# Kernel tuning notes

Hardware: AMD Instinct MI355X
Metric: run time of the kernel (lower is better)

The kernel has to match this reference:

```python
import jax, jax.numpy as jnp
import numpy as np

WEIGHT_CE = 1.0
WEIGHT_DICE = 1.0
EPS = 1e-10
SMOOTH = 1e-5


def setup_inputs() -> dict:
    key = jax.random.key(0)
    k1, k2 = jax.random.split(key)
    B, N, H, W, D = 2, 8, 128, 128, 128
    logits = jax.random.normal(k1, (B, N, H, W, D), dtype=jnp.float32)
    pred = jax.nn.softmax(logits, axis=1)  # module expects softmaxed preds
    target = jax.random.randint(k2, (B, 1, H, W, D), 0, N, dtype=jnp.int32)
    return {"pred": pred, "target": target}


def reference(pred, target):
    # pred: (B, N, H, W, D) softmax probs; target: (B, 1, H, W, D) int labels
    B, N = pred.shape[0], pred.shape[1]
    t = target[:, 0]  # (B, H, W, D)

    # --- CE part (faithful to the original's cross-batch one-hot bug) ---
    # loss[b2, hwd] = -sum_b sum_c 1[t[b2,hwd]==c] * log(pred[b,c,hwd]+eps)
    logp_sum = jnp.sum(jnp.log(pred + EPS), axis=0)  # (N, H, W, D)
    gathered = jnp.take_along_axis(
        jnp.broadcast_to(logp_sum[None], (B,) + logp_sum.shape),
        t[:, None], axis=1)[:, 0]  # (B, H, W, D)
    celoss = -jnp.mean(gathered) / B

    # --- MONAI DiceLoss(softmax=False, to_onehot_y=True), defaults ---
    oh = (t[:, None] == jnp.arange(N, dtype=t.dtype)[None, :, None, None, None]).astype(pred.dtype)  # (B,N,H,W,D)
    inter = jnp.sum(oh * pred, axis=(2, 3, 4))   # (B, N)
    ground_o = jnp.sum(oh, axis=(2, 3, 4))       # (B, N)
    pred_o = jnp.sum(pred, axis=(2, 3, 4))       # (B, N)
    dice = jnp.mean(1.0 - (2.0 * inter + SMOOTH) / (ground_o + pred_o + SMOOTH))

    return WEIGHT_CE * celoss + WEIGHT_DICE * dice
```

## Files before the change

### kernel.cpp

```cpp
#include <hip/hip_runtime.h>

#define S_VOX (128*128*128)
#define QV (S_VOX/4)
#define EPSF 1e-10f
#define SMOOTHF 1e-5f

#define NACC 49

__device__ __forceinline__ float wave_reduce(float v) {
#pragma unroll
    for (int off = 32; off > 0; off >>= 1)
        v += __shfl_down(v, off, 64);
    return v;
}

__global__ __launch_bounds__(256) void dice_main(const float* __restrict__ pred,
                                                 const int* __restrict__ tgt,
                                                 float* __restrict__ ws) {
    const float4* p4 = (const float4*)pred;
    const int4*   t4 = (const int4*)tgt;

    float ce = 0.f;
    float inter[2][8];
    float po[2][8];
    int   gc[2][8];
#pragma unroll
    for (int b = 0; b < 2; b++)
#pragma unroll
        for (int n = 0; n < 8; n++) { inter[b][n] = 0.f; po[b][n] = 0.f; gc[b][n] = 0; }

    const int tid    = blockIdx.x * blockDim.x + threadIdx.x;
    const int stride = gridDim.x * blockDim.x;

    for (int q = tid; q < QV; q += stride) {
        const int4 t0 = t4[q];
        const int4 t1 = t4[QV + q];
#pragma unroll
        for (int n = 0; n < 8; n++) {
            const float4 a = p4[n * QV + q];
            const float4 b = p4[(8 + n) * QV + q];

            po[0][n] += (a.x + a.y) + (a.z + a.w);
            po[1][n] += (b.x + b.y) + (b.z + b.w);

#define VOXEL(pa, pb, ta, tb)                                              \
            {                                                              \
                float lg = __logf((pa) + EPSF) + __logf((pb) + EPSF);      \
                int m0 = ((ta) == n);                                      \
                int m1 = ((tb) == n);                                      \
                ce += lg * (float)(m0 + m1);                               \
                inter[0][n] += m0 ? (pa) : 0.f;                            \
                inter[1][n] += m1 ? (pb) : 0.f;                            \
                gc[0][n] += m0;                                            \
                gc[1][n] += m1;                                            \
            }
            VOXEL(a.x, b.x, t0.x, t1.x)
            VOXEL(a.y, b.y, t0.y, t1.y)
            VOXEL(a.z, b.z, t0.z, t1.z)
            VOXEL(a.w, b.w, t0.w, t1.w)
#undef VOXEL
        }
    }

    float acc[NACC];
    acc[0] = ce;
#pragma unroll
    for (int b = 0; b < 2; b++)
#pragma unroll
        for (int n = 0; n < 8; n++) {
            acc[1  + b * 8 + n] = inter[b][n];
            acc[17 + b * 8 + n] = (float)gc[b][n];
            acc[33 + b * 8 + n] = po[b][n];
        }

    __shared__ float red[4][NACC];
    const int lane = threadIdx.x & 63;
    const int wave = threadIdx.x >> 6;
#pragma unroll
    for (int i = 0; i < NACC; i++) {
        float v = wave_reduce(acc[i]);
        if (lane == 0) red[wave][i] = v;
    }
    __syncthreads();
    if (threadIdx.x < NACC) {
        float s = red[0][threadIdx.x] + red[1][threadIdx.x] +
                  red[2][threadIdx.x] + red[3][threadIdx.x];
        atomicAdd(&ws[threadIdx.x], s);
    }
}

__global__ void dice_finalize(const float* __restrict__ ws, float* __restrict__ out) {
    const int i = threadIdx.x;
    float term = 0.f;
    if (i < 16) {
        float inter = ws[1 + i];
        float g     = ws[17 + i];
        float p     = ws[33 + i];
        term = 1.0f - (2.0f * inter + SMOOTHF) / (g + p + SMOOTHF);
    }
    term = wave_reduce(term);
    if (i == 0) {
        float celoss = -ws[0] / (4.0f * (float)S_VOX);
        out[0] = celoss + term * (1.0f / 16.0f);
    }
}

extern "C" void kernel_launch(void* const* d_in, const int* in_sizes, int n_in,
                              void* d_out, int out_size, void* d_ws, size_t ws_size,
                              hipStream_t stream) {
    const float* pred = (const float*)d_in[0];
    const int*   tgt  = (const int*)d_in[1];
    float* ws  = (float*)d_ws;
    float* out = (float*)d_out;

    hipMemsetAsync(ws, 0, NACC * sizeof(float), stream);
    dice_main<<<1024, 256, 0, stream>>>(pred, tgt, ws);
    dice_finalize<<<1, 64, 0, stream>>>(ws, out);
}
```

Before: 228.4 us.

## Select gathered probabilities before log, one voxel-quad per thread, fuse finalize

Result: slower. 543.6 us (+138.1%).

```diff
diff --git a/kernel.cpp b/kernel.cpp
--- a/kernel.cpp
+++ b/kernel.cpp
@@ -4,104 +4,108 @@
 #define QV (S_VOX/4)
 #define EPSF 1e-10f
 #define SMOOTHF 1e-5f
+#define NACC 49
+#define NBLK 2048
+#define LN2F 0.69314718056f
 
-#define NACC 49
 
-__device__ __forceinline__ float wave_reduce(float v) {
-#pragma unroll
-    for (int off = 32; off > 0; off >>= 1)
-        v += __shfl_down(v, off, 64);
-    return v;
-}
-
-__global__ __launch_bounds__(256) void dice_main(const float* __restrict__ pred,
-                                                 const int* __restrict__ tgt,
-                                                 float* __restrict__ ws) {
+__global__ __launch_bounds__(256, 2) void dice_main(const float* __restrict__ pred,
+                                                    const int* __restrict__ tgt,
+                                                    float* __restrict__ ws,
+                                                    float* __restrict__ out) {
     const float4* p4 = (const float4*)pred;
     const int4*   t4 = (const int4*)tgt;
+    const int q = blockIdx.x * 256 + threadIdx.x;
 
-    float ce = 0.f;
-    float inter[2][8];
-    float po[2][8];
-    int   gc[2][8];
+    const int4 T0 = t4[q];
+    const int4 T1 = t4[QV + q];
+    float4 A[8], B[8];
 #pragma unroll
-    for (int b = 0; b < 2; b++)
+    for (int n = 0; n < 8; n++) A[n] = p4[n * QV + q];
 #pragma unroll
-        for (int n = 0; n < 8; n++) { inter[b][n] = 0.f; po[b][n] = 0.f; gc[b][n] = 0; }
+    for (int n = 0; n < 8; n++) B[n] = p4[(8 + n) * QV + q];
 
-    const int tid    = blockIdx.x * blockDim.x + threadIdx.x;
-    const int stride = gridDim.x * blockDim.x;
+    float i0[8], i1[8], g0[8], g1[8], po0[8], po1[8];
+    float s00x = A[0].x, s00y = A[0].y, s00z = A[0].z, s00w = A[0].w;
+    float s01x = B[0].x, s01y = B[0].y, s01z = B[0].z, s01w = B[0].w;
+    float s10x = A[0].x, s10y = A[0].y, s10z = A[0].z, s10w = A[0].w;
+    float s11x = B[0].x, s11y = B[0].y, s11z = B[0].z, s11w = B[0].w;
 
-    for (int q = tid; q < QV; q += stride) {
-        const int4 t0 = t4[q];
-        const int4 t1 = t4[QV + q];
 #pragma unroll
-        for (int n = 0; n < 8; n++) {
-            const float4 a = p4[n * QV + q];
-            const float4 b = p4[(8 + n) * QV + q];
+    for (int n = 0; n < 8; n++) {
+        const float4 a = A[n];
+        const float4 b = B[n];
+        po0[n] = (a.x + a.y) + (a.z + a.w);
+        po1[n] = (b.x + b.y) + (b.z + b.w);
 
-            po[0][n] += (a.x + a.y) + (a.z + a.w);
-            po[1][n] += (b.x + b.y) + (b.z + b.w);
+        float ii0 = 0.f, ii1 = 0.f, gg0 = 0.f, gg1 = 0.f;
+#define VOX(c)                                                          \
+        {                                                               \
+            const bool m0 = (T0.c == n);                                \
+            const bool m1 = (T1.c == n);                                \
+            if (n > 0) {                                                \
+                s00##c = m0 ? a.c : s00##c;                             \
+                s01##c = m0 ? b.c : s01##c;                             \
+                s10##c = m1 ? a.c : s10##c;                             \
+                s11##c = m1 ? b.c : s11##c;                             \
+            }                                                           \
+            ii0 += m0 ? a.c : 0.f;                                      \
+            ii1 += m1 ? b.c : 0.f;                                      \
+            gg0 += m0 ? 1.f : 0.f;                                      \
+            gg1 += m1 ? 1.f : 0.f;                                      \
+        }
+        VOX(x) VOX(y) VOX(z) VOX(w)
+#undef VOX
+        i0[n] = ii0; i1[n] = ii1; g0[n] = gg0; g1[n] = gg1;
+    }
 
-#define VOXEL(pa, pb, ta, tb)                                              \
-            {                                                              \
-                float lg = __logf((pa) + EPSF) + __logf((pb) + EPSF);      \
-                int m0 = ((ta) == n);                                      \
-                int m1 = ((tb) == n);                                      \
-                ce += lg * (float)(m0 + m1);                               \
-                inter[0][n] += m0 ? (pa) : 0.f;                            \
-                inter[1][n] += m1 ? (pb) : 0.f;                            \
-                gc[0][n] += m0;                                            \
-                gc[1][n] += m1;                                            \
-            }
-            VOXEL(a.x, b.x, t0.x, t1.x)
-            VOXEL(a.y, b.y, t0.y, t1.y)
-            VOXEL(a.z, b.z, t0.z, t1.z)
-            VOXEL(a.w, b.w, t0.w, t1.w)
-#undef VOXEL
-        }
-    }
+    const float ce = LN2F *
+        ( (__log2f(s00x + EPSF) + __log2f(s01x + EPSF) + __log2f(s10x + EPSF) + __log2f(s11x + EPSF))
+        + (__log2f(s00y + EPSF) + __log2f(s01y + EPSF) + __log2f(s10y + EPSF) + __log2f(s11y + EPSF))
+        + (__log2f(s00z + EPSF) + __log2f(s01z + EPSF) + __log2f(s10z + EPSF) + __log2f(s11z + EPSF))
+        + (__log2f(s00w + EPSF) + __log2f(s01w + EPSF) + __log2f(s10w + EPSF) + __log2f(s11w + EPSF)) );
 
     float acc[NACC];
     acc[0] = ce;
 #pragma unroll
-    for (int b = 0; b < 2; b++)
-#pragma unroll
-        for (int n = 0; n < 8; n++) {
-            acc[1  + b * 8 + n] = inter[b][n];
-            acc[17 + b * 8 + n] = (float)gc[b][n];
-            acc[33 + b * 8 + n] = po[b][n];
-        }
+    for (int n = 0; n < 8; n++) {
+        acc[1  + n] = i0[n];  acc[9  + n] = i1[n];
+        acc[17 + n] = g0[n];  acc[25 + n] = g1[n];
+        acc[33 + n] = po0[n]; acc[41 + n] = po1[n];
+    }
 
-    __shared__ float red[4][NACC];
+    __shared__ float lds[64 * 53];
     const int lane = threadIdx.x & 63;
     const int wave = threadIdx.x >> 6;
 #pragma unroll
     for (int i = 0; i < NACC; i++) {
-        float v = wave_reduce(acc[i]);
-        if (lane == 0) red[wave][i] = v;
+        float v = acc[i];
+        v += __shfl_down(v, 32, 64);
+        v += __shfl_down(v, 16, 64);
+        if (lane < 16) lds[(wave * 16 + lane) * 53 + i] = v;
     }
     __syncthreads();
     if (threadIdx.x < NACC) {
-        float s = red[0][threadIdx.x] + red[1][threadIdx.x] +
-                  red[2][threadIdx.x] + red[3][threadIdx.x];
+        float s = 0.f;
+#pragma unroll
+        for (int k = 0; k < 64; k++) s += lds[k * 53 + threadIdx.x];
         atomicAdd(&ws[threadIdx.x], s);
     }
-}
 
-__global__ void dice_finalize(const float* __restrict__ ws, float* __restrict__ out) {
-    const int i = threadIdx.x;
-    float term = 0.f;
-    if (i < 16) {
-        float inter = ws[1 + i];
-        float g     = ws[17 + i];
-        float p     = ws[33 + i];
-        term = 1.0f - (2.0f * inter + SMOOTHF) / (g + p + SMOOTHF);
-    }
-    term = wave_reduce(term);
-    if (i == 0) {
-        float celoss = -ws[0] / (4.0f * (float)S_VOX);
-        out[0] = celoss + term * (1.0f / 16.0f);
+    __threadfence();
+    __syncthreads();
+    if (threadIdx.x == 0) {
+        const unsigned prev = atomicAdd((unsigned int*)(ws + NACC), 1u);
+        if (prev == (unsigned)(gridDim.x - 1)) {
+            float v[NACC];
+#pragma unroll
+            for (int i = 0; i < NACC; i++) v[i] = atomicAdd(&ws[i], 0.0f);
+            float dice = 0.f;
+#pragma unroll
+            for (int k = 0; k < 16; k++)
+                dice += 1.0f - (2.0f * v[1 + k] + SMOOTHF) / (v[17 + k] + v[33 + k] + SMOOTHF);
+            out[0] = -v[0] / (4.0f * (float)S_VOX) + dice * (1.0f / 16.0f);
+        }
     }
 }
 
@@ -113,7 +117,6 @@
     float* ws  = (float*)d_ws;
     float* out = (float*)d_out;
 
-    hipMemsetAsync(ws, 0, NACC * sizeof(float), stream);
-    dice_main<<<1024, 256, 0, stream>>>(pred, tgt, ws);
-    dice_finalize<<<1, 64, 0, stream>>>(ws, out);
+    hipMemsetAsync(ws, 0, (NACC + 1) * sizeof(float), stream);
+    dice_main<<<NBLK, 256, 0, stream>>>(pred, tgt, ws, out);
 }
```
